# Performance work log

Hardware: AMD Instinct MI355X
Metric: run time of the kernel (lower is better)

Reference implementation:

```python
import jax, jax.numpy as jnp
import numpy as np
import math

B, P, L, LMAX = 8, 64, 32, 2048
IN_DIM, TE_DIM = 12, 20
POINT = IN_DIM + TE_DIM  # 32
HID = 128
TTCN = HID - 1  # 127
NHEAD = 4
NLAYER = 2
DFF = 2048  # torch TransformerEncoderLayer default dim_feedforward
NQ = 5
TAU = 300.0
DELTA = 5.0 * 60.0  # delta_minutes=5 -> seconds


def _pe_table(M, D):
    pos = np.arange(M, dtype=np.float32)[:, None]
    div = np.exp(np.arange(0, D, 2, dtype=np.float32) * (-math.log(10000.0) / D))
    pe = np.zeros((M, D), np.float32)
    pe[:, 0::2] = np.sin(pos * div)
    pe[:, 1::2] = np.cos(pos * div)
    return jnp.asarray(pe)


def _time_bias(M):
    idx = np.arange(M, dtype=np.float32)
    dist = np.abs(idx[:, None] - idx[None, :]) * DELTA
    return jnp.asarray(np.log(np.exp(-dist / TAU) + 1e-12).astype(np.float32))


def _ln(x, g, b):
    m = jnp.mean(x, axis=-1, keepdims=True)
    v = jnp.var(x, axis=-1, keepdims=True)
    return (x - m) * jax.lax.rsqrt(v + 1e-5) * g + b


def _mha(qx, kx, vx, Wq, bq, Wk, bk, Wv, bv, Wo, bo, bias=None, key_pad=None):
    Bq, Mq, D = qx.shape
    Mk = kx.shape[1]
    dh = D // NHEAD
    q = (qx @ Wq + bq).reshape(Bq, Mq, NHEAD, dh).transpose(0, 2, 1, 3)
    k = (kx @ Wk + bk).reshape(Bq, Mk, NHEAD, dh).transpose(0, 2, 1, 3)
    v = (vx @ Wv + bv).reshape(Bq, Mk, NHEAD, dh).transpose(0, 2, 1, 3)
    s = jnp.einsum('bhqd,bhkd->bhqk', q, k) / math.sqrt(dh)
    if bias is not None:
        s = s + bias[None, None]
    if key_pad is not None:
        s = jnp.where(key_pad[:, None, None, :], -1e9, s)
    a = jax.nn.softmax(s, axis=-1)
    o = jnp.einsum('bhqk,bhkd->bhqd', a, v).transpose(0, 2, 1, 3).reshape(Bq, Mq, D)
    return o @ Wo + bo


def forward_fn(data_sequence, ts_sequence, patch_mask, patch_index, num_batch,
               te_scale_W, te_scale_b, te_per_W, te_per_b,
               fg_W1, fg_b1, fg_W2, fg_b2, fg_W3, fg_b3, T_bias,
               ga_Wq, ga_bq, ga_Wk, ga_bk, ga_Wv, ga_bv, ga_Wo, ga_bo,
               tf_Wq, tf_bq, tf_Wk, tf_bk, tf_Wv, tf_bv, tf_Wo, tf_bo,
               tf_ln1_g, tf_ln1_b, tf_ff_W1, tf_ff_b1, tf_ff_W2, tf_ff_b2,
               tf_ln2_g, tf_ln2_b,
               cls_query, cls_Wq, cls_bq, cls_Wk, cls_bk, cls_Wv, cls_bv,
               cls_Wo, cls_bo, cls_out_W, cls_out_b):
    # --- patchify_by_len, vectorized: per-patch lengths -> cumsum starts + gather ---
    mvalid = patch_mask > 0
    lens = jnp.where(mvalid, jnp.maximum(patch_index, 0), 0)
    starts = jnp.cumsum(lens, axis=1) - lens  # exclusive cumsum (B,P)
    lar = jnp.arange(L)
    idx = starts[:, :, None] + lar[None, None, :]  # (B,P,L)
    valid = (lar[None, None, :] < lens[:, :, None]) & (idx < num_batch[:, None, None]) & mvalid[:, :, None]
    idx_c = jnp.clip(idx, 0, LMAX - 1).reshape(B, P * L)
    Xg = jnp.take_along_axis(data_sequence, idx_c[:, :, None], axis=1).reshape(B, P, L, IN_DIM)
    tsg = jnp.take_along_axis(ts_sequence, idx_c, axis=1).reshape(B, P, L, 1)
    mask_pt = valid.astype(jnp.float32)[..., None]  # (B,P,L,1)
    X_patch = Xg * mask_pt
    ts_patch = tsg * mask_pt
    # --- LearnableTE ---
    te = jnp.concatenate([ts_patch @ te_scale_W + te_scale_b,
                          jnp.sin(ts_patch @ te_per_W + te_per_b)], axis=-1)
    X_int = jnp.concatenate([X_patch, te], axis=-1).reshape(B * P, L, POINT)
    mask2 = mask_pt.reshape(B * P, L, 1)
    # --- TTCN: MLP-generated dynamic filters, masked softmax over timesteps ---
    h = jax.nn.relu(X_int @ fg_W1 + fg_b1)
    h = jax.nn.relu(h @ fg_W2 + fg_b2)
    Filt = h @ fg_W3 + fg_b3  # (N, L, TTCN*POINT)
    Fm = Filt * mask2 + (1.0 - mask2) * -1e8
    Fs = jax.nn.softmax(Fm, axis=1).reshape(B * P, L, TTCN, POINT)
    ttcn = jnp.einsum('nlp,nltp->nt', X_int, Fs)
    h_t = jax.nn.relu(ttcn + T_bias)
    patch_exists = (jnp.sum(mask2, axis=1) > 0).astype(jnp.float32)  # (N,1)
    x = jnp.concatenate([h_t, patch_exists], axis=-1).reshape(B, P, HID)
    # --- stacked time-biased patch attention + transformer encoder ---
    tb = _time_bias(P)
    pe = _pe_table(P, HID)
    key_pad = patch_mask <= 0
    pm = patch_mask[:, :, None]
    for l in range(NLAYER):
        x_last = x
        ga = _mha(x, x, x, ga_Wq[l], ga_bq[l], ga_Wk[l], ga_bk[l],
                  ga_Wv[l], ga_bv[l], ga_Wo[l], ga_bo[l], bias=tb, key_pad=key_pad)
        x = x + ga * pm
        x = x + pe[None]
        # post-norm TransformerEncoderLayer, tf_layer=1, dropout=0 at inference
        a = _mha(x, x, x, tf_Wq[l], tf_bq[l], tf_Wk[l], tf_bk[l],
                 tf_Wv[l], tf_bv[l], tf_Wo[l], tf_bo[l])
        x = _ln(x + a, tf_ln1_g[l], tf_ln1_b[l])
        f = jax.nn.relu(x @ tf_ff_W1[l] + tf_ff_b1[l]) @ tf_ff_W2[l] + tf_ff_b2[l]
        x = _ln(x + f, tf_ln2_g[l], tf_ln2_b[l])
        x = x_last + x
        x = x * pm
    # --- 5-query cross-attention classifier ---
    q = jnp.broadcast_to(cls_query[None], (B, NQ, HID))
    z = _mha(q, x, x, cls_Wq, cls_bq, cls_Wk, cls_bk, cls_Wv, cls_bv,
             cls_Wo, cls_bo, key_pad=key_pad)
    logits = (z @ cls_out_W + cls_out_b)[..., 0]  # (B,5)
    return logits


def setup_inputs() -> dict:
    key = jax.random.key(0)
    ks = iter(jax.random.split(key, 64))
    def nrm(shape, s=0.05):
        return (jax.random.normal(next(ks), shape) * s).astype(jnp.float32)
    inp = {}
    inp['data_sequence'] = jax.random.normal(next(ks), (B, LMAX, IN_DIM), dtype=jnp.float32)
    inp['ts_sequence'] = jax.random.uniform(next(ks), (B, LMAX), dtype=jnp.float32) * 100.0
    inp['patch_mask'] = jnp.ones((B, P), jnp.float32)
    inp['patch_index'] = jax.random.randint(next(ks), (B, P), 1, L + 1)
    inp['num_batch'] = jnp.full((B,), LMAX, jnp.int32)
    inp['te_scale_W'] = nrm((1, 1), 0.5)
    inp['te_scale_b'] = nrm((1,), 0.5)
    inp['te_per_W'] = nrm((1, TE_DIM - 1), 0.5)
    inp['te_per_b'] = nrm((TE_DIM - 1,), 0.5)
    inp['fg_W1'] = nrm((POINT, TTCN)); inp['fg_b1'] = jnp.zeros((TTCN,), jnp.float32)
    inp['fg_W2'] = nrm((TTCN, TTCN)); inp['fg_b2'] = jnp.zeros((TTCN,), jnp.float32)
    inp['fg_W3'] = nrm((TTCN, POINT * TTCN)); inp['fg_b3'] = jnp.zeros((POINT * TTCN,), jnp.float32)
    inp['T_bias'] = nrm((1, TTCN), 0.5)
    for nm in ['ga_Wq', 'ga_Wk', 'ga_Wv', 'ga_Wo', 'tf_Wq', 'tf_Wk', 'tf_Wv', 'tf_Wo']:
        inp[nm] = nrm((NLAYER, HID, HID))
    for nm in ['ga_bq', 'ga_bk', 'ga_bv', 'ga_bo', 'tf_bq', 'tf_bk', 'tf_bv', 'tf_bo', 'tf_ff_b2']:
        inp[nm] = jnp.zeros((NLAYER, HID), jnp.float32)
    inp['tf_ln1_g'] = jnp.ones((NLAYER, HID), jnp.float32)
    inp['tf_ln1_b'] = jnp.zeros((NLAYER, HID), jnp.float32)
    inp['tf_ln2_g'] = jnp.ones((NLAYER, HID), jnp.float32)
    inp['tf_ln2_b'] = jnp.zeros((NLAYER, HID), jnp.float32)
    inp['tf_ff_W1'] = nrm((NLAYER, HID, DFF))
    inp['tf_ff_b1'] = jnp.zeros((NLAYER, DFF), jnp.float32)
    inp['tf_ff_W2'] = nrm((NLAYER, DFF, HID))
    inp['cls_query'] = nrm((NQ, HID), 0.5)
    for nm in ['cls_Wq', 'cls_Wk', 'cls_Wv', 'cls_Wo']:
        inp[nm] = nrm((HID, HID))
    for nm in ['cls_bq', 'cls_bk', 'cls_bv', 'cls_bo']:
        inp[nm] = jnp.zeros((HID,), jnp.float32)
    inp['cls_out_W'] = nrm((HID, 1))
    inp['cls_out_b'] = jnp.zeros((1,), jnp.float32)
    return inp


def reference(data_sequence, ts_sequence, patch_mask, patch_index, num_batch,
              te_scale_W, te_scale_b, te_per_W, te_per_b,
              fg_W1, fg_b1, fg_W2, fg_b2, fg_W3, fg_b3, T_bias,
              ga_Wq, ga_bq, ga_Wk, ga_bk, ga_Wv, ga_bv, ga_Wo, ga_bo,
              tf_Wq, tf_bq, tf_Wk, tf_bk, tf_Wv, tf_bv, tf_Wo, tf_bo,
              tf_ln1_g, tf_ln1_b, tf_ff_W1, tf_ff_b1, tf_ff_W2, tf_ff_b2,
              tf_ln2_g, tf_ln2_b,
              cls_query, cls_Wq, cls_bq, cls_Wk, cls_bk, cls_Wv, cls_bv,
              cls_Wo, cls_bo, cls_out_W, cls_out_b):
    return forward_fn(data_sequence, ts_sequence, patch_mask, patch_index, num_batch,
                      te_scale_W, te_scale_b, te_per_W, te_per_b,
                      fg_W1, fg_b1, fg_W2, fg_b2, fg_W3, fg_b3, T_bias,
                      ga_Wq, ga_bq, ga_Wk, ga_bk, ga_Wv, ga_bv, ga_Wo, ga_bo,
                      tf_Wq, tf_bq, tf_Wk, tf_bk, tf_Wv, tf_bv, tf_Wo, tf_bo,
                      tf_ln1_g, tf_ln1_b, tf_ff_W1, tf_ff_b1, tf_ff_W2, tf_ff_b2,
                      tf_ln2_g, tf_ln2_b,
                      cls_query, cls_Wq, cls_bq, cls_Wk, cls_bk, cls_Wv, cls_bv,
                      cls_Wo, cls_bo, cls_out_W, cls_out_b)
```

## Files before the change

kernel.cpp:

```cpp
#include <hip/hip_runtime.h>
#include <math.h>

#define BB 8
#define PP 64
#define LL 32
#define LMAXX 2048
#define INDIM 12
#define PNT 32
#define HIDD 128
#define TTCNN 127
#define NPATCH 512

#define EPI_NONE 0
#define EPI_RELU 1
#define EPI_GA   2
#define EPI_LN   3
#define EPI_LNF  4

typedef __attribute__((ext_vector_type(8))) short short8v;
typedef __attribute__((ext_vector_type(4))) float float4v;

__device__ inline unsigned short f2bf(float f) {
    unsigned int u = __float_as_uint(f);
    unsigned int r = (u + 0x7FFFu + ((u >> 16) & 1u)) >> 16;
    return (unsigned short)r;
}

__global__ void tables_kernel(float* __restrict__ tb, float* __restrict__ pe)
{
    int e = blockIdx.x*256 + threadIdx.x;
    if (e < 64*64) {
        int i = e >> 6, j = e & 63;
        float dist = fabsf((float)(i - j)) * (300.0f / 300.0f);
        tb[e] = logf(expf(-dist) + 1e-12f);
    } else if (e < 64*64 + 64*128) {
        int e2 = e - 64*64;
        int i = e2 >> 7, d = e2 & 127;
        int mm = d >> 1;
        float div = expf((float)(2*mm) * (-logf(10000.f)/128.f));
        float ang = (float)i * div;
        pe[e2] = (d & 1) ? cosf(ang) : sinf(ang);
    }
}

__global__ void w3t_kernel(const float* __restrict__ W3, unsigned short* __restrict__ W3TB)
{
    int e = blockIdx.x*256 + threadIdx.x;
    if (e >= 4096*128) return;
    int kk = e >> 12, cidx = e & 4095;
    float v = (kk < TTCNN && cidx < 4064) ? W3[kk*4064 + cidx] : 0.f;
    W3TB[cidx*128 + kk] = f2bf(v);
}

__global__ void prep_h2_kernel(const float* __restrict__ data, const float* __restrict__ ts,
                               const float* __restrict__ pmask, const int* __restrict__ pindex,
                               const int* __restrict__ nbatch,
                               const float* __restrict__ teW, const float* __restrict__ teB,
                               const float* __restrict__ tePW, const float* __restrict__ tePB,
                               const float* __restrict__ W1, const float* __restrict__ b1,
                               const float* __restrict__ W2, const float* __restrict__ b2,
                               float* __restrict__ xint, float* __restrict__ maskout,
                               unsigned short* __restrict__ h2o)
{
    int n = blockIdx.x;
    int b = n >> 6, p = n & 63;
    __shared__ int s_start, s_len;
    __shared__ float s_mk[LL];
    __shared__ alignas(16) float Xs[LL*36];
    __shared__ alignas(16) float H1[LL*128];
    int tid = threadIdx.x;
    if (tid == 0) {
        int start = 0;
        for (int j = 0; j < p; ++j) {
            float mv = pmask[b*PP + j];
            int pi = pindex[b*PP + j];
            start += (mv > 0.f) ? (pi > 0 ? pi : 0) : 0;
        }
        float mvp = pmask[b*PP + p];
        int pip = pindex[b*PP + p];
        s_len = (mvp > 0.f) ? (pip > 0 ? pip : 0) : 0;
        s_start = start;
    }
    __syncthreads();
    int start = s_start, len = s_len, nb2 = nbatch[b];
    if (tid < LL) {
        int l = tid;
        int idx = start + l;
        float v = (l < len && idx < nb2) ? 1.f : 0.f;
        s_mk[l] = v;
        maskout[n*LL + l] = v;
    }
    __syncthreads();
    for (int e = tid; e < LL*PNT; e += 128) {
        int l = e >> 5, d = e & 31;
        float mv = s_mk[l];
        int idx = start + l;
        if (idx < 0) idx = 0;
        if (idx > LMAXX-1) idx = LMAXX-1;
        float val;
        if (d < INDIM) {
            val = (mv > 0.f) ? data[(b*LMAXX + idx)*INDIM + d] : 0.f;
        } else {
            float tsm = (mv > 0.f) ? ts[b*LMAXX + idx] : 0.f;
            if (d == INDIM) val = tsm * teW[0] + teB[0];
            else { int j = d - INDIM - 1; val = sinf(tsm * tePW[j] + tePB[j]); }
        }
        Xs[l*36 + d] = val;
        xint[n*(LL*PNT) + e] = val;
    }
    __syncthreads();
    int j = tid;
    float acc[LL];
    if (j < TTCNN) {
        #pragma unroll
        for (int l = 0; l < LL; ++l) acc[l] = b1[j];
        for (int d4 = 0; d4 < 8; ++d4) {
            float w0 = W1[(d4*4+0)*TTCNN + j];
            float w1 = W1[(d4*4+1)*TTCNN + j];
            float w2 = W1[(d4*4+2)*TTCNN + j];
            float w3 = W1[(d4*4+3)*TTCNN + j];
            #pragma unroll
            for (int l = 0; l < LL; ++l) {
                float4 x = *(float4*)&Xs[l*36 + d4*4];
                acc[l] = fmaf(x.x, w0, acc[l]);
                acc[l] = fmaf(x.y, w1, acc[l]);
                acc[l] = fmaf(x.z, w2, acc[l]);
                acc[l] = fmaf(x.w, w3, acc[l]);
            }
        }
        #pragma unroll
        for (int l = 0; l < LL; ++l) H1[l*128 + j] = fmaxf(acc[l], 0.f);
    } else {
        #pragma unroll
        for (int l = 0; l < LL; ++l) H1[l*128 + 127] = 0.f;
    }
    __syncthreads();
    if (j < TTCNN) {
        #pragma unroll
        for (int l = 0; l < LL; ++l) acc[l] = b2[j];
        for (int k4 = 0; k4 < 32; ++k4) {
            int k = k4*4;
            float w0 = W2[(k+0)*TTCNN + j];
            float w1 = W2[(k+1)*TTCNN + j];
            float w2 = W2[(k+2)*TTCNN + j];
            float w3 = (k+3 < TTCNN) ? W2[(k+3)*TTCNN + j] : 0.f;
            #pragma unroll
            for (int l = 0; l < LL; ++l) {
                float4 h = *(float4*)&H1[l*128 + k];
                acc[l] = fmaf(h.x, w0, acc[l]);
                acc[l] = fmaf(h.y, w1, acc[l]);
                acc[l] = fmaf(h.z, w2, acc[l]);
                acc[l] = fmaf(h.w, w3, acc[l]);
            }
        }
        #pragma unroll
        for (int l = 0; l < LL; ++l) h2o[(n*LL + l)*128 + j] = f2bf(fmaxf(acc[l], 0.f));
    } else {
        #pragma unroll
        for (int l = 0; l < LL; ++l) h2o[(n*LL + l)*128 + 127] = 0;
    }
}

__global__ __launch_bounds__(256) void ttcn_mfma_kernel(
    const unsigned short* __restrict__ h2b,
    const float* __restrict__ xint,
    const float* __restrict__ mask,
    const unsigned short* __restrict__ w3tb,
    const float* __restrict__ b3,
    const float* __restrict__ tbias,
    float* __restrict__ x)
{
    int bid = blockIdx.x;
    int n = bid >> 3, chunk = bid & 7;
    __shared__ alignas(16) unsigned short h2s[32*136];
    __shared__ alignas(16) float Xs[32*36];
    __shared__ float mk[32];
    int tid = threadIdx.x;
    for (int f = tid; f < 512; f += 256) {
        int l = f >> 4, c16 = f & 15;
        *(short8v*)&h2s[l*136 + c16*8] = *(const short8v*)&h2b[(n*32 + l)*128 + c16*8];
    }
    {
        int l = tid >> 3, d4 = (tid & 7)*4;
        *(float4*)&Xs[l*36 + d4] = *(const float4*)&xint[n*1024 + l*32 + d4];
    }
    if (tid < 32) mk[tid] = mask[n*32 + tid];
    __syncthreads();
    if (chunk == 0 && tid == 0) {
        float e = 0.f;
        for (int l = 0; l < 32; ++l) e += mk[l];
        x[n*HIDD + 127] = (e > 0.f) ? 1.f : 0.f;
    }
    int wave = tid >> 6, lane = tid & 63;
    int li = lane & 15, hi = lane >> 4;
    short8v a[2][4];
    #pragma unroll
    for (int mt = 0; mt < 2; ++mt)
        #pragma unroll
        for (int kk = 0; kk < 4; ++kk)
            a[mt][kk] = *(short8v*)&h2s[(mt*16 + li)*136 + kk*32 + hi*8];
    int cwbase = chunk*512 + wave*128;
    for (int tl = 0; tl < 4; ++tl) {
        int c0 = cwbase + tl*32;
        float4v acc[2][2] = {};
        #pragma unroll
        for (int nt2 = 0; nt2 < 2; ++nt2) {
            const unsigned short* bp = &w3tb[(size_t)(c0 + nt2*16 + li)*128 + hi*8];
            #pragma unroll
            for (int kk = 0; kk < 4; ++kk) {
                short8v bf = *(const short8v*)&bp[kk*32];
                acc[0][nt2] = __builtin_amdgcn_mfma_f32_16x16x32_bf16(a[0][kk], bf, acc[0][nt2], 0, 0, 0);
                acc[1][nt2] = __builtin_amdgcn_mfma_f32_16x16x32_bf16(a[1][kk], bf, acc[1][nt2], 0, 0, 0);
            }
        }
        int t = c0 >> 5;
        float colv2 = 0.f;
        #pragma unroll
        for (int nt2 = 0; nt2 < 2; ++nt2) {
            int c = c0 + nt2*16 + li;
            float bv = (c < 4064) ? b3[c] : 0.f;
            int p = (nt2 << 4) + li;
            float fm[8];
            #pragma unroll
            for (int mt = 0; mt < 2; ++mt)
                #pragma unroll
                for (int r4 = 0; r4 < 4; ++r4) {
                    int r = mt*16 + hi*4 + r4;
                    float mv = mk[r];
                    fm[mt*4 + r4] = (acc[mt][nt2][r4] + bv)*mv + (1.f - mv)*(-1e8f);
                }
            float m = fm[0];
            #pragma unroll
            for (int i = 1; i < 8; ++i) m = fmaxf(m, fm[i]);
            m = fmaxf(m, __shfl_xor(m, 16));
            m = fmaxf(m, __shfl_xor(m, 32));
            float s = 0.f, w = 0.f;
            #pragma unroll
            for (int mt = 0; mt < 2; ++mt)
                #pragma unroll
                for (int r4 = 0; r4 < 4; ++r4) {
                    int r = mt*16 + hi*4 + r4;
                    float e = expf(fm[mt*4 + r4] - m);
                    s += e;
                    w += e * Xs[r*36 + p];
                }
            s += __shfl_xor(s, 16); w += __shfl_xor(w, 16);
            s += __shfl_xor(s, 32); w += __shfl_xor(w, 32);
            colv2 += w / s;
        }
        colv2 += __shfl_xor(colv2, 1);
        colv2 += __shfl_xor(colv2, 2);
        colv2 += __shfl_xor(colv2, 4);
        colv2 += __shfl_xor(colv2, 8);
        if (lane == 0 && t < TTCNN)
            x[n*HIDD + t] = fmaxf(colv2 + tbias[t], 0.f);
    }
}

__global__ __launch_bounds__(256) void lin_kernel(
    const float* __restrict__ A, int lda,
    const float* __restrict__ W0, const float* __restrict__ Wb0,
    const float* __restrict__ W1, const float* __restrict__ Wb1,
    const float* __restrict__ W2, const float* __restrict__ Wb2,
    float* __restrict__ O0, float* __restrict__ O1, float* __restrict__ O2,
    int M, int K, int N, int epi,
    const float* __restrict__ xres, const float* __restrict__ xlast_in,
    float* __restrict__ xlast_out,
    const float* __restrict__ pmk, const float* __restrict__ pe,
    const float* __restrict__ g, const float* __restrict__ bt)
{
    __shared__ alignas(16) float As[8*68];
    __shared__ float red[4][4][2];
    int tid = threadIdx.x;
    int cloc = tid & 127, rh = tid >> 7;
    int c = blockIdx.z*128 + cloc;
    int r0 = blockIdx.x*8;
    const float* W; const float* Wb; float* O;
    if (blockIdx.y == 0)      { W = W0; Wb = Wb0; O = O0; }
    else if (blockIdx.y == 1) { W = W1; Wb = Wb1; O = O1; }
    else                      { W = W2; Wb = Wb2; O = O2; }
    float acc0 = 0.f, acc1 = 0.f, acc2 = 0.f, acc3 = 0.f;
    for (int kc = 0; kc < K; kc += 64) {
        __syncthreads();
        if (tid < 128) {
            int row = tid >> 4, kk = (tid & 15)*4;
            int r = r0 + row;
            float4 v = make_float4(0.f, 0.f, 0.f, 0.f);
            if (r < M) v = *(const float4*)&A[(size_t)r*lda + kc + kk];
            *(float4*)&As[row*68 + kk] = v;
        }
        __syncthreads();
        const float* wp = &W[(size_t)kc*N + c];
        #pragma unroll 4
        for (int kk4 = 0; kk4 < 16; ++kk4) {
            float w0 = wp[(size_t)(kk4*4+0)*N];
            float w1 = wp[(size_t)(kk4*4+1)*N];
            float w2 = wp[(size_t)(kk4*4+2)*N];
            float w3 = wp[(size_t)(kk4*4+3)*N];
            float4 a0 = *(float4*)&As[(rh*4+0)*68 + kk4*4];
            float4 a1 = *(float4*)&As[(rh*4+1)*68 + kk4*4];
            float4 a2 = *(float4*)&As[(rh*4+2)*68 + kk4*4];
            float4 a3 = *(float4*)&As[(rh*4+3)*68 + kk4*4];
            acc0 += a0.x*w0 + a0.y*w1 + a0.z*w2 + a0.w*w3;
            acc1 += a1.x*w0 + a1.y*w1 + a1.z*w2 + a1.w*w3;
            acc2 += a2.x*w0 + a2.y*w1 + a2.z*w2 + a2.w*w3;
            acc3 += a3.x*w0 + a3.y*w1 + a3.z*w2 + a3.w*w3;
        }
    }
    float bv = Wb ? Wb[c] : 0.f;
    float val[4] = {acc0 + bv, acc1 + bv, acc2 + bv, acc3 + bv};
    int rbase = r0 + rh*4;
    if (epi == EPI_NONE || epi == EPI_RELU) {
        #pragma unroll
        for (int i = 0; i < 4; ++i) {
            int r = rbase + i;
            if (r < M) {
                float v = val[i];
                if (epi == EPI_RELU) v = fmaxf(v, 0.f);
                O[(size_t)r*N + c] = v;
            }
        }
    } else if (epi == EPI_GA) {
        #pragma unroll
        for (int i = 0; i < 4; ++i) {
            int r = rbase + i;
            float xr = xres[r*128 + cloc];
            float pmv = pmk[r];
            float pev = pe[(r & 63)*128 + cloc];
            xlast_out[r*128 + cloc] = xr;
            O[r*128 + cloc] = xr + val[i]*pmv + pev;
        }
    } else {
        float tv[4], s[4], s2[4];
        #pragma unroll
        for (int i = 0; i < 4; ++i) {
            int r = rbase + i;
            tv[i] = xres[r*128 + cloc] + val[i];
            s[i] = tv[i];
            s2[i] = tv[i]*tv[i];
        }
        #pragma unroll
        for (int i = 0; i < 4; ++i) {
            for (int off = 32; off >= 1; off >>= 1) {
                s[i]  += __shfl_xor(s[i],  off);
                s2[i] += __shfl_xor(s2[i], off);
            }
        }
        int wid = tid >> 6;
        if ((tid & 63) == 0) {
            #pragma unroll
            for (int i = 0; i < 4; ++i) { red[wid][i][0] = s[i]; red[wid][i][1] = s2[i]; }
        }
        __syncthreads();
        int pw = wid ^ 1;
        #pragma unroll
        for (int i = 0; i < 4; ++i) {
            float st  = red[wid][i][0] + red[pw][i][0];
            float s2t = red[wid][i][1] + red[pw][i][1];
            float mean = st * (1.f/128.f);
            float var = s2t * (1.f/128.f) - mean*mean;
            float rs = rsqrtf(var + 1e-5f);
            float y = (tv[i] - mean)*rs*g[cloc] + bt[cloc];
            int r = rbase + i;
            if (epi == EPI_LN) O[r*128 + cloc] = y;
            else               O[r*128 + cloc] = (xlast_in[r*128 + cloc] + y)*pmk[r];
        }
    }
}

__global__ __launch_bounds__(256) void ff2_partial_kernel(
    const float* __restrict__ A,
    const float* __restrict__ W,
    float* __restrict__ PART)
{
    __shared__ alignas(16) float As[8*68];
    int tid = threadIdx.x;
    int cloc = tid & 127, rh = tid >> 7;
    int r0 = blockIdx.x*8;
    int kz = blockIdx.z*256;
    float acc0 = 0.f, acc1 = 0.f, acc2 = 0.f, acc3 = 0.f;
    for (int kc = kz; kc < kz + 256; kc += 64) {
        __syncthreads();
        if (tid < 128) {
            int row = tid >> 4, kk = (tid & 15)*4;
            *(float4*)&As[row*68 + kk] = *(const float4*)&A[(size_t)(r0+row)*2048 + kc + kk];
        }
        __syncthreads();
        const float* wp = &W[(size_t)kc*128 + cloc];
        #pragma unroll 4
        for (int kk4 = 0; kk4 < 16; ++kk4) {
            float w0 = wp[(size_t)(kk4*4+0)*128];
            float w1 = wp[(size_t)(kk4*4+1)*128];
            float w2 = wp[(size_t)(kk4*4+2)*128];
            float w3 = wp[(size_t)(kk4*4+3)*128];
            float4 a0 = *(float4*)&As[(rh*4+0)*68 + kk4*4];
            float4 a1 = *(float4*)&As[(rh*4+1)*68 + kk4*4];
            float4 a2 = *(float4*)&As[(rh*4+2)*68 + kk4*4];
            float4 a3 = *(float4*)&As[(rh*4+3)*68 + kk4*4];
            acc0 += a0.x*w0 + a0.y*w1 + a0.z*w2 + a0.w*w3;
            acc1 += a1.x*w0 + a1.y*w1 + a1.z*w2 + a1.w*w3;
            acc2 += a2.x*w0 + a2.y*w1 + a2.z*w2 + a2.w*w3;
            acc3 += a3.x*w0 + a3.y*w1 + a3.z*w2 + a3.w*w3;
        }
    }
    float* pb = &PART[((size_t)blockIdx.z*512 + r0 + rh*4)*128 + cloc];
    pb[0]     = acc0;
    pb[128]   = acc1;
    pb[256]   = acc2;
    pb[384]   = acc3;
}

__global__ void ln2f_kernel(const float* __restrict__ PART, const float* __restrict__ b2,
                            const float* __restrict__ xres, const float* __restrict__ xlast,
                            const float* __restrict__ pmk,
                            const float* __restrict__ g, const float* __restrict__ bt,
                            float* __restrict__ xout)
{
    int r = blockIdx.x, c = threadIdx.x;
    float v = b2[c];
    #pragma unroll
    for (int z = 0; z < 8; ++z) v += PART[((size_t)z*512 + r)*128 + c];
    float tv = xres[r*128 + c] + v;
    float s = tv, s2 = tv*tv;
    for (int off = 32; off >= 1; off >>= 1) {
        s  += __shfl_xor(s,  off);
        s2 += __shfl_xor(s2, off);
    }
    __shared__ float red[2][2];
    int w = c >> 6;
    if ((c & 63) == 0) { red[w][0] = s; red[w][1] = s2; }
    __syncthreads();
    float st  = red[0][0] + red[1][0];
    float s2t = red[0][1] + red[1][1];
    float mean = st * (1.f/128.f);
    float var = s2t * (1.f/128.f) - mean*mean;
    float y = (tv - mean)*rsqrtf(var + 1e-5f)*g[c] + bt[c];
    xout[r*128 + c] = (xlast[r*128 + c] + y)*pmk[r];
}

__global__ __launch_bounds__(256) void attn_kernel(
    const float* __restrict__ q, const float* __restrict__ k, const float* __restrict__ v,
    float* __restrict__ out, const float* __restrict__ tb,
    const float* __restrict__ pmk, int flags)
{
    int bid = blockIdx.x;
    int b = bid >> 3, h = (bid >> 1) & 3, half = bid & 1;
    int rbase = half*32;
    __shared__ alignas(16) float qs[32*36];
    __shared__ alignas(16) float ks[64*36];
    __shared__ alignas(16) float vs[64*36];
    __shared__ float as_[32*68];
    int tid = threadIdx.x;
    {
        int m = tid >> 3, d4 = (tid & 7)*4;
        *(float4*)&qs[m*36 + d4] = *(const float4*)&q[(b*64 + rbase + m)*128 + h*32 + d4];
    }
    for (int f = tid; f < 512; f += 256) {
        int m = f >> 3, d4 = (f & 7)*4;
        int gofs = (b*64 + m)*128 + h*32 + d4;
        *(float4*)&ks[m*36 + d4] = *(const float4*)&k[gofs];
        *(float4*)&vs[m*36 + d4] = *(const float4*)&v[gofs];
    }
    __syncthreads();
    int r = tid >> 3, qd = tid & 7;
    float sreg[8];
    #pragma unroll
    for (int j = 0; j < 8; ++j) {
        int cc = j*8 + qd;
        float acc = 0.f;
        #pragma unroll
        for (int d4 = 0; d4 < 8; ++d4) {
            float4 a = *(float4*)&qs[r*36 + d4*4];
            float4 bb = *(float4*)&ks[cc*36 + d4*4];
            acc += a.x*bb.x + a.y*bb.y + a.z*bb.z + a.w*bb.w;
        }
        float s = acc * 0.17677669529663687f;
        if (flags & 1) s += tb[(rbase + r)*64 + cc];
        if (flags & 2) { if (pmk[b*64 + cc] <= 0.f) s = -1e9f; }
        sreg[j] = s;
    }
    float m = sreg[0];
    #pragma unroll
    for (int j = 1; j < 8; ++j) m = fmaxf(m, sreg[j]);
    m = fmaxf(m, __shfl_xor(m, 1));
    m = fmaxf(m, __shfl_xor(m, 2));
    m = fmaxf(m, __shfl_xor(m, 4));
    float ssum = 0.f;
    #pragma unroll
    for (int j = 0; j < 8; ++j) { sreg[j] = expf(sreg[j] - m); ssum += sreg[j]; }
    ssum += __shfl_xor(ssum, 1);
    ssum += __shfl_xor(ssum, 2);
    ssum += __shfl_xor(ssum, 4);
    float inv = 1.f / ssum;
    #pragma unroll
    for (int j = 0; j < 8; ++j) as_[r*68 + j*8 + qd] = sreg[j]*inv;
    __syncthreads();
    float o0 = 0.f, o1 = 0.f, o2 = 0.f, o3 = 0.f;
    int d0 = qd*4;
    for (int cc = 0; cc < 64; ++cc) {
        float a = as_[r*68 + cc];
        float4 v4 = *(float4*)&vs[cc*36 + d0];
        o0 += a*v4.x; o1 += a*v4.y; o2 += a*v4.z; o3 += a*v4.w;
    }
    *(float4*)&out[(b*64 + rbase + r)*128 + h*32 + d0] = make_float4(o0, o1, o2, o3);
}

__global__ __launch_bounds__(256) void cls_attn_kernel(
    const float* __restrict__ clsq, const float* __restrict__ Wq, const float* __restrict__ bq,
    const float* __restrict__ k, const float* __restrict__ v,
    const float* __restrict__ pmk,
    const float* __restrict__ Wo, const float* __restrict__ bo,
    const float* __restrict__ WoutW, const float* __restrict__ boutB,
    float* __restrict__ outp)
{
    int b = blockIdx.x;
    __shared__ alignas(16) float ks[64*132];
    __shared__ alignas(16) float vs[64*132];
    __shared__ alignas(16) float q5[5*132];
    __shared__ float cq[5*128];
    __shared__ float sb[5*68];
    __shared__ float z[5*132];
    __shared__ float wef[129];
    int tid = threadIdx.x;
    for (int f = tid; f < 64*32; f += 256) {
        int m = f >> 5, d4 = (f & 31)*4;
        *(float4*)&ks[m*132 + d4] = *(const float4*)&k[(b*64+m)*128 + d4];
        *(float4*)&vs[m*132 + d4] = *(const float4*)&v[(b*64+m)*128 + d4];
    }
    for (int e = tid; e < 5*128; e += 256) {
        cq[e] = clsq[e];
        z[(e >> 7)*132 + (e & 127)] = 0.f;
    }
    __syncthreads();
    for (int it = tid; it < 5*128; it += 256) {
        int qr = it >> 7, d = it & 127;
        float a = bq[d];
        for (int kk = 0; kk < 128; ++kk) a += cq[qr*128 + kk]*Wq[kk*128 + d];
        q5[qr*132 + d] = a;
    }
    if (tid < 128) {
        float s = 0.f;
        for (int cc = 0; cc < 128; ++cc) s += Wo[tid*128 + cc]*WoutW[cc];
        wef[tid] = s;
    } else if (tid == 128) {
        float t = boutB[0];
        for (int cc = 0; cc < 128; ++cc) t += bo[cc]*WoutW[cc];
        wef[128] = t;
    }
    __syncthreads();
    for (int h = 0; h < 4; ++h) {
        for (int it = tid; it < 5*64; it += 256) {
            int qr = it >> 6, cc = it & 63;
            float acc = 0.f;
            #pragma unroll
            for (int d4 = 0; d4 < 8; ++d4) {
                float4 a = *(float4*)&q5[qr*132 + h*32 + d4*4];
                float4 bb = *(float4*)&ks[cc*132 + h*32 + d4*4];
                acc += a.x*bb.x + a.y*bb.y + a.z*bb.z + a.w*bb.w;
            }
            float s = acc * 0.17677669529663687f;
            if (pmk[b*64 + cc] <= 0.f) s = -1e9f;
            sb[qr*68 + cc] = s;
        }
        __syncthreads();
        if (tid < 5) {
            float m = -3e38f;
            for (int cc = 0; cc < 64; ++cc) m = fmaxf(m, sb[tid*68 + cc]);
            float ssum = 0.f;
            for (int cc = 0; cc < 64; ++cc) {
                float e = expf(sb[tid*68 + cc] - m);
                sb[tid*68 + cc] = e;
                ssum += e;
            }
            float inv = 1.f/ssum;
            for (int cc = 0; cc < 64; ++cc) sb[tid*68 + cc] *= inv;
        }
        __syncthreads();
        for (int it = tid; it < 5*32; it += 256) {
            int qr = it >> 5, d = it & 31;
            float acc = 0.f;
            for (int cc = 0; cc < 64; ++cc) acc += sb[qr*68 + cc]*vs[cc*132 + h*32 + d];
            z[qr*132 + h*32 + d] = acc;
        }
        __syncthreads();
    }
    if (tid < 5) {
        float acc = wef[128];
        for (int d = 0; d < 128; ++d) acc += z[tid*132 + d]*wef[d];
        outp[b*5 + tid] = acc;
    }
}

extern "C" void kernel_launch(void* const* d_in, const int* in_sizes, int n_in,
                              void* d_out, int out_size, void* d_ws, size_t ws_size,
                              hipStream_t stream)
{
    (void)n_in; (void)out_size; (void)ws_size;
    #define FP(i) ((const float*)d_in[i])
    const float* data = FP(0);
    const float* ts   = FP(1);
    const float* pmask= FP(2);
    const int*   pidx = (const int*)d_in[3];
    const int*   nb   = (const int*)d_in[4];
    const float* teW  = FP(5);
    const float* teB  = FP(6);
    const float* tePW = FP(7);
    const float* tePB = FP(8);
    const float* fgW1 = FP(9);
    const float* fgb1 = FP(10);
    const float* fgW2 = FP(11);
    const float* fgb2 = FP(12);
    const float* fgW3 = FP(13);
    const float* fgb3 = FP(14);
    const float* Tb   = FP(15);
    const float *gaWq,*gaWk,*gaWv,*gaWo,*tfWq,*tfWk,*tfWv,*tfWo;
    const float *gabq,*gabk,*gabv,*gabo,*tfbq,*tfbk,*tfbv,*tfbo,*ffb2;
    const float *ln1g,*ln1b,*ln2g,*ln2b,*ffW1,*ffb1,*ffW2;
    const float *clsq,*clsWq,*clsWk,*clsWv,*clsWo,*clsbq,*clsbk,*clsbv,*clsbo,*cloW,*clob;
    if (in_sizes[17] == 2*128*128) {
        gaWq=FP(16); gaWk=FP(17); gaWv=FP(18); gaWo=FP(19);
        tfWq=FP(20); tfWk=FP(21); tfWv=FP(22); tfWo=FP(23);
        gabq=FP(24); gabk=FP(25); gabv=FP(26); gabo=FP(27);
        tfbq=FP(28); tfbk=FP(29); tfbv=FP(30); tfbo=FP(31);
        ffb2=FP(32); ln1g=FP(33); ln1b=FP(34); ln2g=FP(35); ln2b=FP(36);
        ffW1=FP(37); ffb1=FP(38); ffW2=FP(39);
        clsq=FP(40); clsWq=FP(41); clsWk=FP(42); clsWv=FP(43); clsWo=FP(44);
        clsbq=FP(45); clsbk=FP(46); clsbv=FP(47); clsbo=FP(48); cloW=FP(49); clob=FP(50);
    } else {
        gaWq=FP(16); gabq=FP(17); gaWk=FP(18); gabk=FP(19);
        gaWv=FP(20); gabv=FP(21); gaWo=FP(22); gabo=FP(23);
        tfWq=FP(24); tfbq=FP(25); tfWk=FP(26); tfbk=FP(27);
        tfWv=FP(28); tfbv=FP(29); tfWo=FP(30); tfbo=FP(31);
        ln1g=FP(32); ln1b=FP(33); ffW1=FP(34); ffb1=FP(35); ffW2=FP(36); ffb2=FP(37);
        ln2g=FP(38); ln2b=FP(39);
        clsq=FP(40); clsWq=FP(41); clsbq=FP(42); clsWk=FP(43); clsbk=FP(44);
        clsWv=FP(45); clsbv=FP(46); clsWo=FP(47); clsbo=FP(48); cloW=FP(49); clob=FP(50);
    }

    float* ws   = (float*)d_ws;
    float* XINT = ws;
    float* PART = ws;
    float* MASK = ws + 524288;
    unsigned short* W3TB = (unsigned short*)(ws + 540672);
    unsigned short* H2Bb = (unsigned short*)(ws + 1060864);
    float* X    = ws + 3158016;
    float* XLAST= X + 65536;
    float* Q    = XLAST + 65536;
    float* Kb   = Q + 65536;
    float* Vb   = Kb + 65536;
    float* ATT  = Vb + 65536;
    float* HIDB = ATT + 65536;
    float* TBT  = HIDB + 1048576;
    float* PET  = TBT + 4096;

    tables_kernel<<<48, 256, 0, stream>>>(TBT, PET);
    w3t_kernel<<<2048, 256, 0, stream>>>(fgW3, W3TB);
    prep_h2_kernel<<<512, 128, 0, stream>>>(data, ts, pmask, pidx, nb, teW, teB, tePW, tePB,
                                            fgW1, fgb1, fgW2, fgb2, XINT, MASK, H2Bb);
    ttcn_mfma_kernel<<<4096, 256, 0, stream>>>(H2Bb, XINT, MASK, W3TB, fgb3, Tb, X);

    for (int l = 0; l < 2; ++l) {
        const float* Wq = gaWq + l*16384; const float* bq = gabq + l*128;
        const float* Wk = gaWk + l*16384; const float* bk = gabk + l*128;
        const float* Wv = gaWv + l*16384; const float* bv = gabv + l*128;
        const float* Wo = gaWo + l*16384; const float* bo = gabo + l*128;
        lin_kernel<<<dim3(64,3,1), 256, 0, stream>>>(X, 128, Wq,bq, Wk,bk, Wv,bv, Q,Kb,Vb,
            512,128,128, EPI_NONE, nullptr,nullptr,nullptr,nullptr,nullptr,nullptr,nullptr);
        attn_kernel<<<64, 256, 0, stream>>>(Q, Kb, Vb, ATT, TBT, pmask, 3);
        lin_kernel<<<dim3(64,1,1), 256, 0, stream>>>(ATT, 128, Wo,bo, Wo,bo, Wo,bo, X,X,X,
            512,128,128, EPI_GA, X, nullptr, XLAST, pmask, PET, nullptr, nullptr);
        const float* Wq2 = tfWq + l*16384; const float* bq2 = tfbq + l*128;
        const float* Wk2 = tfWk + l*16384; const float* bk2 = tfbk + l*128;
        const float* Wv2 = tfWv + l*16384; const float* bv2 = tfbv + l*128;
        const float* Wo2 = tfWo + l*16384; const float* bo2 = tfbo + l*128;
        lin_kernel<<<dim3(64,3,1), 256, 0, stream>>>(X, 128, Wq2,bq2, Wk2,bk2, Wv2,bv2, Q,Kb,Vb,
            512,128,128, EPI_NONE, nullptr,nullptr,nullptr,nullptr,nullptr,nullptr,nullptr);
        attn_kernel<<<64, 256, 0, stream>>>(Q, Kb, Vb, ATT, TBT, pmask, 0);
        lin_kernel<<<dim3(64,1,1), 256, 0, stream>>>(ATT, 128, Wo2,bo2, Wo2,bo2, Wo2,bo2, X,X,X,
            512,128,128, EPI_LN, X, nullptr, nullptr, nullptr, nullptr, ln1g + l*128, ln1b + l*128);
        lin_kernel<<<dim3(64,1,16), 256, 0, stream>>>(X, 128,
            ffW1 + (size_t)l*128*2048, ffb1 + l*2048, ffW1, ffb1, ffW1, ffb1, HIDB,HIDB,HIDB,
            512,128,2048, EPI_RELU, nullptr,nullptr,nullptr,nullptr,nullptr,nullptr,nullptr);
        ff2_partial_kernel<<<dim3(64,1,8), 256, 0, stream>>>(HIDB, ffW2 + (size_t)l*2048*128, PART);
        ln2f_kernel<<<512, 128, 0, stream>>>(PART, ffb2 + l*128, X, XLAST, pmask,
                                             ln2g + l*128, ln2b + l*128, X);
    }

    lin_kernel<<<dim3(64,2,1), 256, 0, stream>>>(X, 128, clsWk,clsbk, clsWv,clsbv, clsWv,clsbv,
        Kb,Vb,Vb, 512,128,128, EPI_NONE, nullptr,nullptr,nullptr,nullptr,nullptr,nullptr,nullptr);
    cls_attn_kernel<<<8, 256, 0, stream>>>(clsq, clsWq, clsbq, Kb, Vb, pmask,
                                           clsWo, clsbo, cloW, clob, (float*)d_out);
}
```

Measured before the change: 458.6 us.

## Retile linear kernels to 32-column blocks, split LN, and simplify TTCN softmax

Replaces the 128-column linear and FF2 kernels with 32-column variants that launch four times more blocks. Each thread now computes one output from a full-K shared tile. LayerNorm 1 moves out of the GEMM epilogue into its own kernel, which adds a launch but lets the Wo projection run across more blocks. The TTCN softmax drops the max-subtraction pass, uses a -30 mask offset, __expf and a hardware reciprocal, and hoists the mask and X values into registers. This risks overflow if logits get large and changes masked-row semantics. The attention kernels also switch to fast exp and reciprocal.

```diff
diff --git a/kernel.cpp b/kernel.cpp
--- a/kernel.cpp
+++ b/kernel.cpp
@@ -14,8 +14,7 @@
 #define EPI_NONE 0
 #define EPI_RELU 1
 #define EPI_GA   2
-#define EPI_LN   3
-#define EPI_LNF  4
+#define EPI_ADD  3
 
 typedef __attribute__((ext_vector_type(8))) short short8v;
 typedef __attribute__((ext_vector_type(4))) float float4v;
@@ -199,6 +198,19 @@
         #pragma unroll
         for (int kk = 0; kk < 4; ++kk)
             a[mt][kk] = *(short8v*)&h2s[(mt*16 + li)*136 + kk*32 + hi*8];
+    float mkr[8], off8[8], xv0[8], xv1[8];
+    #pragma unroll
+    for (int mt = 0; mt < 2; ++mt)
+        #pragma unroll
+        for (int r4 = 0; r4 < 4; ++r4) {
+            int i = mt*4 + r4;
+            int rr = mt*16 + hi*4 + r4;
+            float mv = mk[rr];
+            mkr[i] = mv;
+            off8[i] = (1.f - mv) * (-30.f);
+            xv0[i] = Xs[rr*36 + li];
+            xv1[i] = Xs[rr*36 + 16 + li];
+        }
     int cwbase = chunk*512 + wave*128;
     for (int tl = 0; tl < 4; ++tl) {
         int c0 = cwbase + tl*32;
@@ -217,36 +229,22 @@
         float colv2 = 0.f;
         #pragma unroll
         for (int nt2 = 0; nt2 < 2; ++nt2) {
-            int c = c0 + nt2*16 + li;
-            float bv = (c < 4064) ? b3[c] : 0.f;
-            int p = (nt2 << 4) + li;
-            float fm[8];
-            #pragma unroll
-            for (int mt = 0; mt < 2; ++mt)
-                #pragma unroll
-                for (int r4 = 0; r4 < 4; ++r4) {
-                    int r = mt*16 + hi*4 + r4;
-                    float mv = mk[r];
-                    fm[mt*4 + r4] = (acc[mt][nt2][r4] + bv)*mv + (1.f - mv)*(-1e8f);
-                }
-            float m = fm[0];
-            #pragma unroll
-            for (int i = 1; i < 8; ++i) m = fmaxf(m, fm[i]);
-            m = fmaxf(m, __shfl_xor(m, 16));
-            m = fmaxf(m, __shfl_xor(m, 32));
+            int cglob = c0 + nt2*16 + li;
+            float bv = (cglob < 4064) ? b3[cglob] : 0.f;
             float s = 0.f, w = 0.f;
             #pragma unroll
             for (int mt = 0; mt < 2; ++mt)
                 #pragma unroll
                 for (int r4 = 0; r4 < 4; ++r4) {
-                    int r = mt*16 + hi*4 + r4;
-                    float e = expf(fm[mt*4 + r4] - m);
+                    int i = mt*4 + r4;
+                    float fm = (acc[mt][nt2][r4] + bv)*mkr[i] + off8[i];
+                    float e = __expf(fm);
                     s += e;
-                    w += e * Xs[r*36 + p];
+                    w = fmaf(e, (nt2 == 0) ? xv0[i] : xv1[i], w);
                 }
             s += __shfl_xor(s, 16); w += __shfl_xor(w, 16);
             s += __shfl_xor(s, 32); w += __shfl_xor(w, 32);
-            colv2 += w / s;
+            colv2 = fmaf(w, __builtin_amdgcn_rcpf(s), colv2);
         }
         colv2 += __shfl_xor(colv2, 1);
         colv2 += __shfl_xor(colv2, 2);
@@ -257,157 +255,119 @@
     }
 }
 
-__global__ __launch_bounds__(256) void lin_kernel(
+__global__ __launch_bounds__(256) void lin32_kernel(
     const float* __restrict__ A, int lda,
-    const float* __restrict__ W0, const float* __restrict__ Wb0,
-    const float* __restrict__ W1, const float* __restrict__ Wb1,
-    const float* __restrict__ W2, const float* __restrict__ Wb2,
+    const float* __restrict__ W0, const float* __restrict__ b0,
+    const float* __restrict__ W1, const float* __restrict__ b1,
+    const float* __restrict__ W2, const float* __restrict__ b2,
     float* __restrict__ O0, float* __restrict__ O1, float* __restrict__ O2,
-    int M, int K, int N, int epi,
-    const float* __restrict__ xres, const float* __restrict__ xlast_in,
-    float* __restrict__ xlast_out,
-    const float* __restrict__ pmk, const float* __restrict__ pe,
-    const float* __restrict__ g, const float* __restrict__ bt)
-{
-    __shared__ alignas(16) float As[8*68];
-    __shared__ float red[4][4][2];
+    int K, int N, int epi,
+    const float* __restrict__ xres, float* __restrict__ xlast_out,
+    const float* __restrict__ pmk, const float* __restrict__ pe)
+{
+    __shared__ alignas(16) float As[8][132];
     int tid = threadIdx.x;
-    int cloc = tid & 127, rh = tid >> 7;
-    int c = blockIdx.z*128 + cloc;
-    int r0 = blockIdx.x*8;
+    int r = tid >> 5, c = tid & 31;
+    int row = blockIdx.x*8 + r;
+    int col = blockIdx.z*32 + c;
     const float* W; const float* Wb; float* O;
-    if (blockIdx.y == 0)      { W = W0; Wb = Wb0; O = O0; }
-    else if (blockIdx.y == 1) { W = W1; Wb = Wb1; O = O1; }
-    else                      { W = W2; Wb = Wb2; O = O2; }
-    float acc0 = 0.f, acc1 = 0.f, acc2 = 0.f, acc3 = 0.f;
-    for (int kc = 0; kc < K; kc += 64) {
+    if (blockIdx.y == 0)      { W = W0; Wb = b0; O = O0; }
+    else if (blockIdx.y == 1) { W = W1; Wb = b1; O = O1; }
+    else                      { W = W2; Wb = b2; O = O2; }
+    float a0 = 0.f, a1 = 0.f, a2 = 0.f, a3 = 0.f;
+    for (int kc = 0; kc < K; kc += 128) {
         __syncthreads();
-        if (tid < 128) {
-            int row = tid >> 4, kk = (tid & 15)*4;
-            int r = r0 + row;
-            float4 v = make_float4(0.f, 0.f, 0.f, 0.f);
-            if (r < M) v = *(const float4*)&A[(size_t)r*lda + kc + kk];
-            *(float4*)&As[row*68 + kk] = v;
+        {
+            int lr = tid >> 5, f4 = (tid & 31)*4;
+            *(float4*)&As[lr][f4] = *(const float4*)&A[(size_t)(blockIdx.x*8 + lr)*lda + kc + f4];
         }
         __syncthreads();
-        const float* wp = &W[(size_t)kc*N + c];
-        #pragma unroll 4
-        for (int kk4 = 0; kk4 < 16; ++kk4) {
-            float w0 = wp[(size_t)(kk4*4+0)*N];
-            float w1 = wp[(size_t)(kk4*4+1)*N];
-            float w2 = wp[(size_t)(kk4*4+2)*N];
-            float w3 = wp[(size_t)(kk4*4+3)*N];
-            float4 a0 = *(float4*)&As[(rh*4+0)*68 + kk4*4];
-            float4 a1 = *(float4*)&As[(rh*4+1)*68 + kk4*4];
-            float4 a2 = *(float4*)&As[(rh*4+2)*68 + kk4*4];
-            float4 a3 = *(float4*)&As[(rh*4+3)*68 + kk4*4];
-            acc0 += a0.x*w0 + a0.y*w1 + a0.z*w2 + a0.w*w3;
-            acc1 += a1.x*w0 + a1.y*w1 + a1.z*w2 + a1.w*w3;
-            acc2 += a2.x*w0 + a2.y*w1 + a2.z*w2 + a2.w*w3;
-            acc3 += a3.x*w0 + a3.y*w1 + a3.z*w2 + a3.w*w3;
-        }
-    }
-    float bv = Wb ? Wb[c] : 0.f;
-    float val[4] = {acc0 + bv, acc1 + bv, acc2 + bv, acc3 + bv};
-    int rbase = r0 + rh*4;
-    if (epi == EPI_NONE || epi == EPI_RELU) {
-        #pragma unroll
-        for (int i = 0; i < 4; ++i) {
-            int r = rbase + i;
-            if (r < M) {
-                float v = val[i];
-                if (epi == EPI_RELU) v = fmaxf(v, 0.f);
-                O[(size_t)r*N + c] = v;
-            }
-        }
+        const float* wp = &W[(size_t)kc*N + col];
+        #pragma unroll
+        for (int k4 = 0; k4 < 32; ++k4) {
+            float4 av = *(float4*)&As[r][k4*4];
+            float w0_ = wp[(size_t)(k4*4+0)*N];
+            float w1_ = wp[(size_t)(k4*4+1)*N];
+            float w2_ = wp[(size_t)(k4*4+2)*N];
+            float w3_ = wp[(size_t)(k4*4+3)*N];
+            a0 = fmaf(av.x, w0_, a0);
+            a1 = fmaf(av.y, w1_, a1);
+            a2 = fmaf(av.z, w2_, a2);
+            a3 = fmaf(av.w, w3_, a3);
+        }
+    }
+    float val = (a0 + a1) + (a2 + a3) + Wb[col];
+    if (epi == EPI_NONE) {
+        O[(size_t)row*N + col] = val;
+    } else if (epi == EPI_RELU) {
+        O[(size_t)row*N + col] = fmaxf(val, 0.f);
     } else if (epi == EPI_GA) {
-        #pragma unroll
-        for (int i = 0; i < 4; ++i) {
-            int r = rbase + i;
-            float xr = xres[r*128 + cloc];
-            float pmv = pmk[r];
-            float pev = pe[(r & 63)*128 + cloc];
-            xlast_out[r*128 + cloc] = xr;
-            O[r*128 + cloc] = xr + val[i]*pmv + pev;
-        }
+        float xr = xres[row*128 + col];
+        float pmv = pmk[row];
+        float pev = pe[(row & 63)*128 + col];
+        xlast_out[row*128 + col] = xr;
+        O[row*128 + col] = xr + val*pmv + pev;
     } else {
-        float tv[4], s[4], s2[4];
-        #pragma unroll
-        for (int i = 0; i < 4; ++i) {
-            int r = rbase + i;
-            tv[i] = xres[r*128 + cloc] + val[i];
-            s[i] = tv[i];
-            s2[i] = tv[i]*tv[i];
-        }
-        #pragma unroll
-        for (int i = 0; i < 4; ++i) {
-            for (int off = 32; off >= 1; off >>= 1) {
-                s[i]  += __shfl_xor(s[i],  off);
-                s2[i] += __shfl_xor(s2[i], off);
-            }
-        }
-        int wid = tid >> 6;
-        if ((tid & 63) == 0) {
-            #pragma unroll
-            for (int i = 0; i < 4; ++i) { red[wid][i][0] = s[i]; red[wid][i][1] = s2[i]; }
-        }
-        __syncthreads();
-        int pw = wid ^ 1;
-        #pragma unroll
-        for (int i = 0; i < 4; ++i) {
-            float st  = red[wid][i][0] + red[pw][i][0];
-            float s2t = red[wid][i][1] + red[pw][i][1];
-            float mean = st * (1.f/128.f);
-            float var = s2t * (1.f/128.f) - mean*mean;
-            float rs = rsqrtf(var + 1e-5f);
-            float y = (tv[i] - mean)*rs*g[cloc] + bt[cloc];
-            int r = rbase + i;
-            if (epi == EPI_LN) O[r*128 + cloc] = y;
-            else               O[r*128 + cloc] = (xlast_in[r*128 + cloc] + y)*pmk[r];
-        }
-    }
-}
-
-__global__ __launch_bounds__(256) void ff2_partial_kernel(
+        O[row*128 + col] = xres[row*128 + col] + val;
+    }
+}
+
+__global__ void ln1_kernel(const float* __restrict__ TMP,
+                           const float* __restrict__ g, const float* __restrict__ bt,
+                           float* __restrict__ xout)
+{
+    int r = blockIdx.x, c = threadIdx.x;
+    float tv = TMP[r*128 + c];
+    float s = tv, s2 = tv*tv;
+    for (int off = 32; off >= 1; off >>= 1) {
+        s  += __shfl_xor(s,  off);
+        s2 += __shfl_xor(s2, off);
+    }
+    __shared__ float red[2][2];
+    int w = c >> 6;
+    if ((c & 63) == 0) { red[w][0] = s; red[w][1] = s2; }
+    __syncthreads();
+    float st  = red[0][0] + red[1][0];
+    float s2t = red[0][1] + red[1][1];
+    float mean = st * (1.f/128.f);
+    float var = s2t * (1.f/128.f) - mean*mean;
+    xout[r*128 + c] = (tv - mean)*rsqrtf(var + 1e-5f)*g[c] + bt[c];
+}
+
+__global__ __launch_bounds__(256) void ff2p32_kernel(
     const float* __restrict__ A,
     const float* __restrict__ W,
     float* __restrict__ PART)
 {
-    __shared__ alignas(16) float As[8*68];
+    __shared__ alignas(16) float As[8][260];
     int tid = threadIdx.x;
-    int cloc = tid & 127, rh = tid >> 7;
-    int r0 = blockIdx.x*8;
-    int kz = blockIdx.z*256;
-    float acc0 = 0.f, acc1 = 0.f, acc2 = 0.f, acc3 = 0.f;
-    for (int kc = kz; kc < kz + 256; kc += 64) {
-        __syncthreads();
-        if (tid < 128) {
-            int row = tid >> 4, kk = (tid & 15)*4;
-            *(float4*)&As[row*68 + kk] = *(const float4*)&A[(size_t)(r0+row)*2048 + kc + kk];
-        }
-        __syncthreads();
-        const float* wp = &W[(size_t)kc*128 + cloc];
-        #pragma unroll 4
-        for (int kk4 = 0; kk4 < 16; ++kk4) {
-            float w0 = wp[(size_t)(kk4*4+0)*128];
-            float w1 = wp[(size_t)(kk4*4+1)*128];
-            float w2 = wp[(size_t)(kk4*4+2)*128];
-            float w3 = wp[(size_t)(kk4*4+3)*128];
-            float4 a0 = *(float4*)&As[(rh*4+0)*68 + kk4*4];
-            float4 a1 = *(float4*)&As[(rh*4+1)*68 + kk4*4];
-            float4 a2 = *(float4*)&As[(rh*4+2)*68 + kk4*4];
-            float4 a3 = *(float4*)&As[(rh*4+3)*68 + kk4*4];
-            acc0 += a0.x*w0 + a0.y*w1 + a0.z*w2 + a0.w*w3;
-            acc1 += a1.x*w0 + a1.y*w1 + a1.z*w2 + a1.w*w3;
-            acc2 += a2.x*w0 + a2.y*w1 + a2.z*w2 + a2.w*w3;
-            acc3 += a3.x*w0 + a3.y*w1 + a3.z*w2 + a3.w*w3;
-        }
-    }
-    float* pb = &PART[((size_t)blockIdx.z*512 + r0 + rh*4)*128 + cloc];
-    pb[0]     = acc0;
-    pb[128]   = acc1;
-    pb[256]   = acc2;
-    pb[384]   = acc3;
+    int r = tid >> 5, c = tid & 31;
+    int ct = blockIdx.z & 3, kz = blockIdx.z >> 2;
+    int row = blockIdx.x*8 + r;
+    int col = ct*32 + c;
+    int k0 = kz*256;
+    {
+        int lr = tid >> 5, f4 = (tid & 31)*4;
+        const float* ap = &A[(size_t)(blockIdx.x*8 + lr)*2048 + k0];
+        *(float4*)&As[lr][f4]       = *(const float4*)&ap[f4];
+        *(float4*)&As[lr][128 + f4] = *(const float4*)&ap[128 + f4];
+    }
+    __syncthreads();
+    const float* wp = &W[(size_t)k0*128 + col];
+    float a0 = 0.f, a1 = 0.f, a2 = 0.f, a3 = 0.f;
+    #pragma unroll 16
+    for (int k4 = 0; k4 < 64; ++k4) {
+        float4 av = *(float4*)&As[r][k4*4];
+        float w0_ = wp[(size_t)(k4*4+0)*128];
+        float w1_ = wp[(size_t)(k4*4+1)*128];
+        float w2_ = wp[(size_t)(k4*4+2)*128];
+        float w3_ = wp[(size_t)(k4*4+3)*128];
+        a0 = fmaf(av.x, w0_, a0);
+        a1 = fmaf(av.y, w1_, a1);
+        a2 = fmaf(av.z, w2_, a2);
+        a3 = fmaf(av.w, w3_, a3);
+    }
+    PART[((size_t)kz*512 + row)*128 + col] = (a0 + a1) + (a2 + a3);
 }
 
 __global__ void ln2f_kernel(const float* __restrict__ PART, const float* __restrict__ b2,
@@ -487,11 +447,11 @@
     m = fmaxf(m, __shfl_xor(m, 4));
     float ssum = 0.f;
     #pragma unroll
-    for (int j = 0; j < 8; ++j) { sreg[j] = expf(sreg[j] - m); ssum += sreg[j]; }
+    for (int j = 0; j < 8; ++j) { sreg[j] = __expf(sreg[j] - m); ssum += sreg[j]; }
     ssum += __shfl_xor(ssum, 1);
     ssum += __shfl_xor(ssum, 2);
     ssum += __shfl_xor(ssum, 4);
-    float inv = 1.f / ssum;
+    float inv = __builtin_amdgcn_rcpf(ssum);
     #pragma unroll
     for (int j = 0; j < 8; ++j) as_[r*68 + j*8 + qd] = sreg[j]*inv;
     __syncthreads();
@@ -568,11 +528,11 @@
             for (int cc = 0; cc < 64; ++cc) m = fmaxf(m, sb[tid*68 + cc]);
             float ssum = 0.f;
             for (int cc = 0; cc < 64; ++cc) {
-                float e = expf(sb[tid*68 + cc] - m);
+                float e = __expf(sb[tid*68 + cc] - m);
                 sb[tid*68 + cc] = e;
                 ssum += e;
             }
-            float inv = 1.f/ssum;
+            float inv = __builtin_amdgcn_rcpf(ssum);
             for (int cc = 0; cc < 64; ++cc) sb[tid*68 + cc] *= inv;
         }
         __syncthreads();
@@ -664,30 +624,31 @@
         const float* Wk = gaWk + l*16384; const float* bk = gabk + l*128;
         const float* Wv = gaWv + l*16384; const float* bv = gabv + l*128;
         const float* Wo = gaWo + l*16384; const float* bo = gabo + l*128;
-        lin_kernel<<<dim3(64,3,1), 256, 0, stream>>>(X, 128, Wq,bq, Wk,bk, Wv,bv, Q,Kb,Vb,
-            512,128,128, EPI_NONE, nullptr,nullptr,nullptr,nullptr,nullptr,nullptr,nullptr);
+        lin32_kernel<<<dim3(64,3,4), 256, 0, stream>>>(X, 128, Wq,bq, Wk,bk, Wv,bv, Q,Kb,Vb,
+            128,128, EPI_NONE, nullptr,nullptr,nullptr,nullptr);
         attn_kernel<<<64, 256, 0, stream>>>(Q, Kb, Vb, ATT, TBT, pmask, 3);
-        lin_kernel<<<dim3(64,1,1), 256, 0, stream>>>(ATT, 128, Wo,bo, Wo,bo, Wo,bo, X,X,X,
-            512,128,128, EPI_GA, X, nullptr, XLAST, pmask, PET, nullptr, nullptr);
+        lin32_kernel<<<dim3(64,1,4), 256, 0, stream>>>(ATT, 128, Wo,bo, Wo,bo, Wo,bo, X,X,X,
+            128,128, EPI_GA, X, XLAST, pmask, PET);
         const float* Wq2 = tfWq + l*16384; const float* bq2 = tfbq + l*128;
         const float* Wk2 = tfWk + l*16384; const float* bk2 = tfbk + l*128;
         const float* Wv2 = tfWv + l*16384; const float* bv2 = tfbv + l*128;
         const float* Wo2 = tfWo + l*16384; const float* bo2 = tfbo + l*128;
-        lin_kernel<<<dim3(64,3,1), 256, 0, stream>>>(X, 128, Wq2,bq2, Wk2,bk2, Wv2,bv2, Q,Kb,Vb,
-            512,128,128, EPI_NONE, nullptr,nullptr,nullptr,nullptr,nullptr,nullptr,nullptr);
+        lin32_kernel<<<dim3(64,3,4), 256, 0, stream>>>(X, 128, Wq2,bq2, Wk2,bk2, Wv2,bv2, Q,Kb,Vb,
+            128,128, EPI_NONE, nullptr,nullptr,nullptr,nullptr);
         attn_kernel<<<64, 256, 0, stream>>>(Q, Kb, Vb, ATT, TBT, pmask, 0);
-        lin_kernel<<<dim3(64,1,1), 256, 0, stream>>>(ATT, 128, Wo2,bo2, Wo2,bo2, Wo2,bo2, X,X,X,
-            512,128,128, EPI_LN, X, nullptr, nullptr, nullptr, nullptr, ln1g + l*128, ln1b + l*128);
-        lin_kernel<<<dim3(64,1,16), 256, 0, stream>>>(X, 128,
+        lin32_kernel<<<dim3(64,1,4), 256, 0, stream>>>(ATT, 128, Wo2,bo2, Wo2,bo2, Wo2,bo2, Q,Q,Q,
+            128,128, EPI_ADD, X, nullptr, nullptr, nullptr);
+        ln1_kernel<<<512, 128, 0, stream>>>(Q, ln1g + l*128, ln1b + l*128, X);
+        lin32_kernel<<<dim3(64,1,64), 256, 0, stream>>>(X, 128,
             ffW1 + (size_t)l*128*2048, ffb1 + l*2048, ffW1, ffb1, ffW1, ffb1, HIDB,HIDB,HIDB,
-            512,128,2048, EPI_RELU, nullptr,nullptr,nullptr,nullptr,nullptr,nullptr,nullptr);
-        ff2_partial_kernel<<<dim3(64,1,8), 256, 0, stream>>>(HIDB, ffW2 + (size_t)l*2048*128, PART);
+            128,2048, EPI_RELU, nullptr,nullptr,nullptr,nullptr);
+        ff2p32_kernel<<<dim3(64,1,32), 256, 0, stream>>>(HIDB, ffW2 + (size_t)l*2048*128, PART);
         ln2f_kernel<<<512, 128, 0, stream>>>(PART, ffb2 + l*128, X, XLAST, pmask,
                                              ln2g + l*128, ln2b + l*128, X);
     }
 
-    lin_kernel<<<dim3(64,2,1), 256, 0, stream>>>(X, 128, clsWk,clsbk, clsWv,clsbv, clsWv,clsbv,
-        Kb,Vb,Vb, 512,128,128, EPI_NONE, nullptr,nullptr,nullptr,nullptr,nullptr,nullptr,nullptr);
+    lin32_kernel<<<dim3(64,2,4), 256, 0, stream>>>(X, 128, clsWk,clsbk, clsWv,clsbv, clsWv,clsbv,
+        Kb,Vb,Vb, 128,128, EPI_NONE, nullptr,nullptr,nullptr,nullptr);
     cls_attn_kernel<<<8, 256, 0, stream>>>(clsq, clsWq, clsbq, Kb, Vb, pmask,
                                            clsWo, clsbo, cloW, clob, (float*)d_out);
 }
```

Measured after the change: 467.7 us. About the same (+2.0%).
